# Kernel tuning notes

Measured on AMD Instinct MI355X. Metric: run time of the kernel, lower is better.

The kernel has to match this reference:

```python
import jax, jax.numpy as jnp
import numpy as np

N, E, D, ED, H, OUT = 10000, 640000, 128, 64, 8, 128  # nodes, edges, node_dim, edge_dim, heads, out_features


def _lin_init(key, out_d, in_d):
    kw, kb = jax.random.split(key)
    lim = 1.0 / np.sqrt(in_d)
    W = jax.random.uniform(kw, (out_d, in_d), jnp.float32, -lim, lim)
    b = jax.random.uniform(kb, (out_d,), jnp.float32, -lim, lim)
    return W, b


def setup_inputs() -> dict:
    key = jax.random.key(0)
    ks = jax.random.split(key, 9)
    h = jax.random.normal(ks[0], (N, D), jnp.float32)
    t_ij = jax.random.normal(ks[1], (E, ED), jnp.float32)
    edge_index = jax.random.randint(ks[2], (2, E), 0, N, dtype=jnp.int64)
    Wq, bq = _lin_init(ks[3], D, D)
    Wk, bk = _lin_init(ks[4], D, D)
    W1, b1 = _lin_init(ks[5], OUT, D)   # MLP layer 1
    W2, b2 = _lin_init(ks[6], OUT, OUT)  # MLP layer 2
    Wre, bre = _lin_init(ks[7], D, ED)
    Wc, bc = _lin_init(ks[8], OUT, OUT)  # combine_heads
    return dict(h=h, t_ij=t_ij, edge_index=edge_index, Wq=Wq, bq=bq, Wk=Wk, bk=bk,
                W1=W1, b1=b1, W2=W2, b2=b2, Wre=Wre, bre=bre, Wc=Wc, bc=bc)


def reference(h, t_ij, edge_index, Wq, bq, Wk, bk, W1, b1, W2, b2, Wre, bre, Wc, bc):
    n_j, n_i = edge_index[0], edge_index[1]
    n_nodes = h.shape[0]
    # projections on nodes, then gather per edge
    q_i = (h @ Wq.T + bq).reshape(n_nodes, H, -1)[n_i]          # [E, H, d_h]
    k_j = (h @ Wk.T + bk).reshape(n_nodes, H, -1)[n_j]          # [E, H, d_h]
    v_nodes = jax.nn.silu(h @ W1.T + b1) @ W2.T + b2            # MLP(h): [N, OUT]
    v_j = v_nodes.reshape(n_nodes, H, -1)[n_j]                  # [E, H, d_h]
    re = jax.nn.silu(t_ij @ Wre.T + bre).reshape(t_ij.shape[0], H, -1)  # [E, H, d_h]
    # per-edge attention logits fused with edge features
    a_ij = (q_i * k_j * re).sum(-1, keepdims=True)              # [E, H, 1]
    # segment softmax grouped by destination node n_i
    m = jax.ops.segment_max(a_ij, n_i, num_segments=n_nodes)
    ex = jnp.exp(a_ij - m[n_i])
    s = jax.ops.segment_sum(ex, n_i, num_segments=n_nodes)
    a_i = ex / (s[n_i] + 1e-16)
    # note: original scales AFTER softmax
    a_i = a_i * (1.0 / np.sqrt(v_j.shape[2]))
    sea_ij = (a_i * v_j).reshape(a_i.shape[0], -1)              # [E, OUT]
    sea_ij = sea_ij @ Wc.T + bc                                 # combine_heads
    return sea_ij
```

## Files before the change

kernel.cpp:

```cpp
#include <hip/hip_runtime.h>

typedef __attribute__((ext_vector_type(8))) _Float16 half8;
typedef __attribute__((ext_vector_type(4))) float floatx4;

#define NN    10000
#define EE    640000
#define DD    128
#define EDD   64
#define HH    8
#define OUTD  128

__device__ __forceinline__ float fast_rcp(float x) { return __builtin_amdgcn_rcpf(x); }

__device__ __forceinline__ half8 cvt8h(const float* __restrict__ p) {
    const floatx4 a = *(const floatx4*)(const void*)p;
    const floatx4 b = *(const floatx4*)(const void*)(p + 4);
    half8 r;
    r[0] = (_Float16)a[0]; r[1] = (_Float16)a[1];
    r[2] = (_Float16)a[2]; r[3] = (_Float16)a[3];
    r[4] = (_Float16)b[0]; r[5] = (_Float16)b[1];
    r[6] = (_Float16)b[2]; r[7] = (_Float16)b[3];
    return r;
}

__device__ __forceinline__ int idx_is64(const int* __restrict__ eidx) {
    return ((eidx[1] | eidx[3] | eidx[5] | eidx[7]) == 0) ? 1 : 0;
}

__global__ void __launch_bounds__(64) k_node(
    const float* __restrict__ h,
    const float* __restrict__ Wq, const float* __restrict__ bq,
    const float* __restrict__ Wk, const float* __restrict__ bk,
    const float* __restrict__ W1, const float* __restrict__ b1,
    const float* __restrict__ W2, const float* __restrict__ b2,
    _Float16* __restrict__ qb, _Float16* __restrict__ kb,
    _Float16* __restrict__ vb, float* __restrict__ sf)
{
    __shared__ _Float16 L[16 * 136];
    const int lane = threadIdx.x;
    const int tile = blockIdx.x;
    const int c16 = lane & 15, q4 = lane >> 4;
    const int m0 = tile * 16;

    const int tid = tile * 64 + lane;
    sf[tid] = 0.0f;
    sf[tid + 40000] = 0.0f;

    const float* hrow = h + (m0 + c16) * DD + q4 * 8;
    half8 af[4];
    af[0] = cvt8h(hrow + 0);
    af[1] = cvt8h(hrow + 32);
    af[2] = cvt8h(hrow + 64);
    af[3] = cvt8h(hrow + 96);

    for (int w = 0; w < 2; ++w) {
        const float* W  = w ? Wk : Wq;
        const float* Bv = w ? bk : bq;
        _Float16* dst   = w ? kb : qb;
        for (int nt = 0; nt < 8; ++nt) {
            const int col = nt * 16 + c16;
            const float bias = Bv[col];
            floatx4 acc = {bias, bias, bias, bias};
            const float* wr = W + col * DD + q4 * 8;
            for (int s = 0; s < 4; ++s)
                acc = __builtin_amdgcn_mfma_f32_16x16x32_f16(
                    af[s], cvt8h(wr + s * 32), acc, 0, 0, 0);
            for (int r = 0; r < 4; ++r)
                dst[(m0 + q4 * 4 + r) * DD + col] = (_Float16)acc[r];
        }
    }

    for (int nt = 0; nt < 8; ++nt) {
        const int col = nt * 16 + c16;
        const float bias = b1[col];
        floatx4 acc = {bias, bias, bias, bias};
        const float* wr = W1 + col * DD + q4 * 8;
        for (int s = 0; s < 4; ++s)
            acc = __builtin_amdgcn_mfma_f32_16x16x32_f16(
                af[s], cvt8h(wr + s * 32), acc, 0, 0, 0);
        for (int r = 0; r < 4; ++r) {
            const float x = acc[r];
            L[(q4 * 4 + r) * 136 + col] = (_Float16)(x * fast_rcp(1.0f + __expf(-x)));
        }
    }
    __syncthreads();

    half8 af2[4];
    const _Float16* l2 = L + c16 * 136 + q4 * 8;
    for (int s = 0; s < 4; ++s)
        af2[s] = *(const half8*)(const void*)(l2 + s * 32);
    for (int nt = 0; nt < 8; ++nt) {
        const int col = nt * 16 + c16;
        const float bias = b2[col];
        floatx4 acc = {bias, bias, bias, bias};
        const float* wr = W2 + col * DD + q4 * 8;
        for (int s = 0; s < 4; ++s)
            acc = __builtin_amdgcn_mfma_f32_16x16x32_f16(
                af2[s], cvt8h(wr + s * 32), acc, 0, 0, 0);
        for (int r = 0; r < 4; ++r)
            vb[(m0 + q4 * 4 + r) * DD + col] = (_Float16)acc[r];
    }
}

__global__ void __launch_bounds__(256) k_logits(
    const float* __restrict__ t, const int* __restrict__ eidx,
    const float* __restrict__ Wre, const float* __restrict__ bre,
    const _Float16* __restrict__ qb, const _Float16* __restrict__ kb,
    float* __restrict__ exf, float* __restrict__ sf)
{
    const int wave = threadIdx.x >> 6;
    const int lane = threadIdx.x & 63;
    const int c16 = lane & 15, q4 = lane >> 4;
    const int tile = blockIdx.x * 4 + wave;
    const int m0 = tile * 16;

    const int is64 = idx_is64(eidx);

    const float* trow = t + (m0 + c16) * EDD + q4 * 8;
    const half8 a0 = cvt8h(trow);
    const half8 a1 = cvt8h(trow + 32);

    int e_r[4], ni_r[4], nj_r[4];
    for (int r = 0; r < 4; ++r) {
        const int e = m0 + q4 * 4 + r;
        e_r[r] = e;
        if (is64) { nj_r[r] = eidx[2 * e];      ni_r[r] = eidx[2 * EE + 2 * e]; }
        else      { nj_r[r] = eidx[e];          ni_r[r] = eidx[EE + e]; }
    }

    for (int nt = 0; nt < 8; ++nt) {
        const int col = nt * 16 + c16;
        const float bias = bre[col];
        floatx4 acc = {bias, bias, bias, bias};
        const float* wr = Wre + col * EDD + q4 * 8;
        acc = __builtin_amdgcn_mfma_f32_16x16x32_f16(a0, cvt8h(wr), acc, 0, 0, 0);
        acc = __builtin_amdgcn_mfma_f32_16x16x32_f16(a1, cvt8h(wr + 32), acc, 0, 0, 0);

        float part[4];
        for (int r = 0; r < 4; ++r) {
            const float x = acc[r];
            const float re = x * fast_rcp(1.0f + __expf(-x));
            const float qv = (float)qb[ni_r[r] * DD + col];
            const float kv = (float)kb[nj_r[r] * DD + col];
            part[r] = re * qv * kv;
        }
        for (int m = 1; m < 16; m <<= 1) {
            part[0] += __shfl_xor(part[0], m, 64);
            part[1] += __shfl_xor(part[1], m, 64);
            part[2] += __shfl_xor(part[2], m, 64);
            part[3] += __shfl_xor(part[3], m, 64);
        }
        if (c16 < 4) {
            const int r = c16;
            const float ex = __expf(part[r]);
            exf[e_r[r] * HH + nt] = ex;
            atomicAdd(&sf[ni_r[r] * HH + nt], ex);
        }
    }
}

__global__ void __launch_bounds__(256) k_out(
    const int* __restrict__ eidx, const float* __restrict__ exf,
    const float* __restrict__ sf, const _Float16* __restrict__ vb,
    const float* __restrict__ Wc, const float* __restrict__ bc,
    float* __restrict__ outp)
{
    __shared__ float Lf[4][16 * 132];
    const int wave = threadIdx.x >> 6;
    const int lane = threadIdx.x & 63;
    const int c16 = lane & 15, q4 = lane >> 4;
    const int tile = blockIdx.x * 4 + wave;
    const int m0 = tile * 16;

    const int is64 = idx_is64(eidx);

    const int e_a = m0 + c16;
    int nj, ni;
    if (is64) { nj = eidx[2 * e_a]; ni = eidx[2 * EE + 2 * e_a]; }
    else      { nj = eidx[e_a];     ni = eidx[EE + e_a]; }

    half8 af[4];
    for (int s = 0; s < 4; ++s) {
        const int h0 = s * 2 + (q4 >> 1);
        const float exv = exf[e_a * HH + h0];
        const float sv = sf[ni * HH + h0];
        const float asc = exv * fast_rcp(sv + 1e-16f) * 0.25f;
        const half8 v8 = *(const half8*)(const void*)(vb + nj * DD + s * 32 + q4 * 8);
        half8 y;
        for (int j = 0; j < 8; ++j)
            y[j] = (_Float16)((float)v8[j] * asc);
        af[s] = y;
    }

    floatx4 acc[8];
    for (int nt = 0; nt < 8; ++nt) {
        const int col = nt * 16 + c16;
        const float bias = bc[col];
        acc[nt] = (floatx4){bias, bias, bias, bias};
        const float* wr = Wc + col * DD + q4 * 8;
        for (int s = 0; s < 4; ++s)
            acc[nt] = __builtin_amdgcn_mfma_f32_16x16x32_f16(
                af[s], cvt8h(wr + s * 32), acc[nt], 0, 0, 0);
    }

    float* Lw = Lf[wave];
    for (int nt = 0; nt < 8; ++nt)
        for (int r = 0; r < 4; ++r)
            Lw[(q4 * 4 + r) * 132 + nt * 16 + c16] = acc[nt][r];
    __syncthreads();

    float* ob = outp + (size_t)m0 * OUTD;
    for (int tt = 0; tt < 8; ++tt) {
        const int idx = tt * 64 + lane;
        const int row = idx >> 5;
        const int c4 = (idx & 31) * 4;
        const floatx4 val = *(const floatx4*)(const void*)&Lw[row * 132 + c4];
        *(floatx4*)(void*)(ob + row * OUTD + c4) = val;
    }
}

extern "C" void kernel_launch(void* const* d_in, const int* in_sizes, int n_in,
                              void* d_out, int out_size, void* d_ws, size_t ws_size,
                              hipStream_t stream) {
    (void)in_sizes; (void)n_in; (void)out_size; (void)ws_size;
    const float* h   = (const float*)d_in[0];
    const float* t   = (const float*)d_in[1];
    const int*   eidx= (const int*)d_in[2];
    const float* Wq  = (const float*)d_in[3];
    const float* bq  = (const float*)d_in[4];
    const float* Wk  = (const float*)d_in[5];
    const float* bk  = (const float*)d_in[6];
    const float* W1  = (const float*)d_in[7];
    const float* b1  = (const float*)d_in[8];
    const float* W2  = (const float*)d_in[9];
    const float* b2  = (const float*)d_in[10];
    const float* Wre = (const float*)d_in[11];
    const float* bre = (const float*)d_in[12];
    const float* Wc  = (const float*)d_in[13];
    const float* bc  = (const float*)d_in[14];
    float* out = (float*)d_out;

    char* ws = (char*)d_ws;
    _Float16* qb = (_Float16*)(ws);
    _Float16* kb = (_Float16*)(ws + 2560000);
    _Float16* vb = (_Float16*)(ws + 5120000);
    float*    exf= (float*)   (ws + 7680000);
    float*    sf = (float*)   (ws + 28160000);

    k_node<<<dim3(625), dim3(64), 0, stream>>>(h, Wq, bq, Wk, bk, W1, b1, W2, b2,
                                               qb, kb, vb, sf);
    k_logits<<<dim3(10000), dim3(256), 0, stream>>>(t, eidx, Wre, bre, qb, kb, exf, sf);
    k_out<<<dim3(10000), dim3(256), 0, stream>>>(eidx, exf, sf, vb, Wc, bc, out);
}
```

Baseline: 1.038 ms.

## Pre-convert weights to fp16, widen node kernel, prefetch q/k gathers, halve out staging

```diff
diff --git a/kernel.cpp b/kernel.cpp
--- a/kernel.cpp
+++ b/kernel.cpp
@@ -27,76 +27,94 @@
     return ((eidx[1] | eidx[3] | eidx[5] | eidx[7]) == 0) ? 1 : 0;
 }
 
-__global__ void __launch_bounds__(64) k_node(
-    const float* __restrict__ h,
-    const float* __restrict__ Wq, const float* __restrict__ bq,
-    const float* __restrict__ Wk, const float* __restrict__ bk,
-    const float* __restrict__ W1, const float* __restrict__ b1,
-    const float* __restrict__ W2, const float* __restrict__ b2,
+__global__ void __launch_bounds__(256) k_prep(
+    const float* __restrict__ Wq, const float* __restrict__ Wk,
+    const float* __restrict__ W1, const float* __restrict__ W2,
+    const float* __restrict__ Wc, const float* __restrict__ Wre,
+    _Float16* __restrict__ w16, float* __restrict__ sf)
+{
+    const int gid = blockIdx.x * 256 + threadIdx.x;
+    float v;
+    if (gid < 16384)      v = Wq[gid];
+    else if (gid < 32768) v = Wk[gid - 16384];
+    else if (gid < 49152) v = W1[gid - 32768];
+    else if (gid < 65536) v = W2[gid - 49152];
+    else if (gid < 81920) v = Wc[gid - 65536];
+    else                  v = Wre[gid - 81920];
+    w16[gid] = (_Float16)v;
+    if (gid < 80000) sf[gid] = 0.0f;
+}
+
+__global__ void __launch_bounds__(512) k_node(
+    const float* __restrict__ h, const _Float16* __restrict__ w16,
+    const float* __restrict__ bq, const float* __restrict__ bk,
+    const float* __restrict__ b1, const float* __restrict__ b2,
     _Float16* __restrict__ qb, _Float16* __restrict__ kb,
-    _Float16* __restrict__ vb, float* __restrict__ sf)
+    _Float16* __restrict__ vb)
 {
     __shared__ _Float16 L[16 * 136];
-    const int lane = threadIdx.x;
-    const int tile = blockIdx.x;
+    const int wave = threadIdx.x >> 6;
+    const int lane = threadIdx.x & 63;
     const int c16 = lane & 15, q4 = lane >> 4;
-    const int m0 = tile * 16;
-
-    const int tid = tile * 64 + lane;
-    sf[tid] = 0.0f;
-    sf[tid + 40000] = 0.0f;
+    const int m0 = blockIdx.x * 16;
+
+    const _Float16* Wq16 = w16;
+    const _Float16* Wk16 = w16 + 16384;
+    const _Float16* W116 = w16 + 32768;
+    const _Float16* W216 = w16 + 49152;
 
     const float* hrow = h + (m0 + c16) * DD + q4 * 8;
     half8 af[4];
-    af[0] = cvt8h(hrow + 0);
+    af[0] = cvt8h(hrow);
     af[1] = cvt8h(hrow + 32);
     af[2] = cvt8h(hrow + 64);
     af[3] = cvt8h(hrow + 96);
 
-    for (int w = 0; w < 2; ++w) {
-        const float* W  = w ? Wk : Wq;
-        const float* Bv = w ? bk : bq;
-        _Float16* dst   = w ? kb : qb;
-        for (int nt = 0; nt < 8; ++nt) {
-            const int col = nt * 16 + c16;
-            const float bias = Bv[col];
-            floatx4 acc = {bias, bias, bias, bias};
-            const float* wr = W + col * DD + q4 * 8;
-            for (int s = 0; s < 4; ++s)
-                acc = __builtin_amdgcn_mfma_f32_16x16x32_f16(
-                    af[s], cvt8h(wr + s * 32), acc, 0, 0, 0);
+#pragma unroll
+    for (int i = 0; i < 3; ++i) {
+        const int u = wave * 3 + i;
+        const int pass = u >> 3;
+        const int nt = u & 7;
+        const _Float16* W = (pass == 0) ? Wq16 : ((pass == 1) ? Wk16 : W116);
+        const float* B    = (pass == 0) ? bq   : ((pass == 1) ? bk   : b1);
+        const int col = nt * 16 + c16;
+        const float bias = B[col];
+        floatx4 acc = {bias, bias, bias, bias};
+        const _Float16* wr = W + col * DD + q4 * 8;
+#pragma unroll
+        for (int s = 0; s < 4; ++s)
+            acc = __builtin_amdgcn_mfma_f32_16x16x32_f16(
+                af[s], *(const half8*)(const void*)(wr + s * 32), acc, 0, 0, 0);
+        if (pass < 2) {
+            _Float16* dst = pass ? kb : qb;
+#pragma unroll
             for (int r = 0; r < 4; ++r)
                 dst[(m0 + q4 * 4 + r) * DD + col] = (_Float16)acc[r];
-        }
-    }
-
-    for (int nt = 0; nt < 8; ++nt) {
-        const int col = nt * 16 + c16;
-        const float bias = b1[col];
+        } else {
+#pragma unroll
+            for (int r = 0; r < 4; ++r) {
+                const float x = acc[r];
+                L[(q4 * 4 + r) * 136 + col] = (_Float16)(x * fast_rcp(1.0f + __expf(-x)));
+            }
+        }
+    }
+    __syncthreads();
+
+    half8 af2[4];
+    const _Float16* l2 = L + c16 * 136 + q4 * 8;
+#pragma unroll
+    for (int s = 0; s < 4; ++s)
+        af2[s] = *(const half8*)(const void*)(l2 + s * 32);
+    {
+        const int col = wave * 16 + c16;
+        const float bias = b2[col];
         floatx4 acc = {bias, bias, bias, bias};
-        const float* wr = W1 + col * DD + q4 * 8;
+        const _Float16* wr = W216 + col * DD + q4 * 8;
+#pragma unroll
         for (int s = 0; s < 4; ++s)
             acc = __builtin_amdgcn_mfma_f32_16x16x32_f16(
-                af[s], cvt8h(wr + s * 32), acc, 0, 0, 0);
-        for (int r = 0; r < 4; ++r) {
-            const float x = acc[r];
-            L[(q4 * 4 + r) * 136 + col] = (_Float16)(x * fast_rcp(1.0f + __expf(-x)));
-        }
-    }
-    __syncthreads();
-
-    half8 af2[4];
-    const _Float16* l2 = L + c16 * 136 + q4 * 8;
-    for (int s = 0; s < 4; ++s)
-        af2[s] = *(const half8*)(const void*)(l2 + s * 32);
-    for (int nt = 0; nt < 8; ++nt) {
-        const int col = nt * 16 + c16;
-        const float bias = b2[col];
-        floatx4 acc = {bias, bias, bias, bias};
-        const float* wr = W2 + col * DD + q4 * 8;
-        for (int s = 0; s < 4; ++s)
-            acc = __builtin_amdgcn_mfma_f32_16x16x32_f16(
-                af2[s], cvt8h(wr + s * 32), acc, 0, 0, 0);
+                af2[s], *(const half8*)(const void*)(wr + s * 32), acc, 0, 0, 0);
+#pragma unroll
         for (int r = 0; r < 4; ++r)
             vb[(m0 + q4 * 4 + r) * DD + col] = (_Float16)acc[r];
     }
@@ -104,7 +122,7 @@
 
 __global__ void __launch_bounds__(256) k_logits(
     const float* __restrict__ t, const int* __restrict__ eidx,
-    const float* __restrict__ Wre, const float* __restrict__ bre,
+    const _Float16* __restrict__ Wre16, const float* __restrict__ bre,
     const _Float16* __restrict__ qb, const _Float16* __restrict__ kb,
     float* __restrict__ exf, float* __restrict__ sf)
 {
@@ -120,29 +138,47 @@
     const half8 a0 = cvt8h(trow);
     const half8 a1 = cvt8h(trow + 32);
 
-    int e_r[4], ni_r[4], nj_r[4];
+    int e_r[4], ni_r[4];
+    const _Float16* qrow[4];
+    const _Float16* krow[4];
+#pragma unroll
     for (int r = 0; r < 4; ++r) {
         const int e = m0 + q4 * 4 + r;
-        e_r[r] = e;
-        if (is64) { nj_r[r] = eidx[2 * e];      ni_r[r] = eidx[2 * EE + 2 * e]; }
-        else      { nj_r[r] = eidx[e];          ni_r[r] = eidx[EE + e]; }
-    }
+        int nj, ni;
+        if (is64) { nj = eidx[2 * e];      ni = eidx[2 * EE + 2 * e]; }
+        else      { nj = eidx[e];          ni = eidx[EE + e]; }
+        e_r[r] = e; ni_r[r] = ni;
+        qrow[r] = qb + ni * DD + c16;
+        krow[r] = kb + nj * DD + c16;
+    }
+
+    _Float16 qv[4], kv[4], qn[4], kn[4];
+#pragma unroll
+    for (int r = 0; r < 4; ++r) { qv[r] = qrow[r][0]; kv[r] = krow[r][0]; }
 
     for (int nt = 0; nt < 8; ++nt) {
+        if (nt < 7) {
+#pragma unroll
+            for (int r = 0; r < 4; ++r) {
+                qn[r] = qrow[r][(nt + 1) * 16];
+                kn[r] = krow[r][(nt + 1) * 16];
+            }
+        }
         const int col = nt * 16 + c16;
         const float bias = bre[col];
         floatx4 acc = {bias, bias, bias, bias};
-        const float* wr = Wre + col * EDD + q4 * 8;
-        acc = __builtin_amdgcn_mfma_f32_16x16x32_f16(a0, cvt8h(wr), acc, 0, 0, 0);
-        acc = __builtin_amdgcn_mfma_f32_16x16x32_f16(a1, cvt8h(wr + 32), acc, 0, 0, 0);
+        const _Float16* wr = Wre16 + col * EDD + q4 * 8;
+        acc = __builtin_amdgcn_mfma_f32_16x16x32_f16(
+            a0, *(const half8*)(const void*)wr, acc, 0, 0, 0);
+        acc = __builtin_amdgcn_mfma_f32_16x16x32_f16(
+            a1, *(const half8*)(const void*)(wr + 32), acc, 0, 0, 0);
 
         float part[4];
+#pragma unroll
         for (int r = 0; r < 4; ++r) {
             const float x = acc[r];
             const float re = x * fast_rcp(1.0f + __expf(-x));
-            const float qv = (float)qb[ni_r[r] * DD + col];
-            const float kv = (float)kb[nj_r[r] * DD + col];
-            part[r] = re * qv * kv;
+            part[r] = re * (float)qv[r] * (float)kv[r];
         }
         for (int m = 1; m < 16; m <<= 1) {
             part[0] += __shfl_xor(part[0], m, 64);
@@ -156,16 +192,18 @@
             exf[e_r[r] * HH + nt] = ex;
             atomicAdd(&sf[ni_r[r] * HH + nt], ex);
         }
-    }
-}
-
-__global__ void __launch_bounds__(256) k_out(
+#pragma unroll
+        for (int r = 0; r < 4; ++r) { qv[r] = qn[r]; kv[r] = kn[r]; }
+    }
+}
+
+__global__ void __launch_bounds__(256, 8) k_out(
     const int* __restrict__ eidx, const float* __restrict__ exf,
     const float* __restrict__ sf, const _Float16* __restrict__ vb,
-    const float* __restrict__ Wc, const float* __restrict__ bc,
+    const _Float16* __restrict__ Wc16, const float* __restrict__ bc,
     float* __restrict__ outp)
 {
-    __shared__ float Lf[4][16 * 132];
+    __shared__ float Lf[4][16 * 68];
     const int wave = threadIdx.x >> 6;
     const int lane = threadIdx.x & 63;
     const int c16 = lane & 15, q4 = lane >> 4;
@@ -180,6 +218,7 @@
     else      { nj = eidx[e_a];     ni = eidx[EE + e_a]; }
 
     half8 af[4];
+#pragma unroll
     for (int s = 0; s < 4; ++s) {
         const int h0 = s * 2 + (q4 >> 1);
         const float exv = exf[e_a * HH + h0];
@@ -187,35 +226,42 @@
         const float asc = exv * fast_rcp(sv + 1e-16f) * 0.25f;
         const half8 v8 = *(const half8*)(const void*)(vb + nj * DD + s * 32 + q4 * 8);
         half8 y;
+#pragma unroll
         for (int j = 0; j < 8; ++j)
             y[j] = (_Float16)((float)v8[j] * asc);
         af[s] = y;
     }
 
     floatx4 acc[8];
+#pragma unroll
     for (int nt = 0; nt < 8; ++nt) {
         const int col = nt * 16 + c16;
         const float bias = bc[col];
         acc[nt] = (floatx4){bias, bias, bias, bias};
-        const float* wr = Wc + col * DD + q4 * 8;
+        const _Float16* wr = Wc16 + col * DD + q4 * 8;
+#pragma unroll
         for (int s = 0; s < 4; ++s)
             acc[nt] = __builtin_amdgcn_mfma_f32_16x16x32_f16(
-                af[s], cvt8h(wr + s * 32), acc[nt], 0, 0, 0);
+                af[s], *(const half8*)(const void*)(wr + s * 32), acc[nt], 0, 0, 0);
     }
 
     float* Lw = Lf[wave];
-    for (int nt = 0; nt < 8; ++nt)
-        for (int r = 0; r < 4; ++r)
-            Lw[(q4 * 4 + r) * 132 + nt * 16 + c16] = acc[nt][r];
-    __syncthreads();
-
     float* ob = outp + (size_t)m0 * OUTD;
-    for (int tt = 0; tt < 8; ++tt) {
-        const int idx = tt * 64 + lane;
-        const int row = idx >> 5;
-        const int c4 = (idx & 31) * 4;
-        const floatx4 val = *(const floatx4*)(const void*)&Lw[row * 132 + c4];
-        *(floatx4*)(void*)(ob + row * OUTD + c4) = val;
+#pragma unroll
+    for (int p = 0; p < 2; ++p) {
+#pragma unroll
+        for (int j = 0; j < 4; ++j)
+#pragma unroll
+            for (int r = 0; r < 4; ++r)
+                Lw[(q4 * 4 + r) * 68 + j * 16 + c16] = acc[p * 4 + j][r];
+#pragma unroll
+        for (int tt = 0; tt < 4; ++tt) {
+            const int idx = tt * 64 + lane;
+            const int row = idx >> 4;
+            const int c4 = (idx & 15) * 4;
+            const floatx4 val = *(const floatx4*)(const void*)&Lw[row * 68 + c4];
+            *(floatx4*)(void*)(ob + row * OUTD + p * 64 + c4) = val;
+        }
     }
 }
 
@@ -246,9 +292,10 @@
     _Float16* vb = (_Float16*)(ws + 5120000);
     float*    exf= (float*)   (ws + 7680000);
     float*    sf = (float*)   (ws + 28160000);
-
-    k_node<<<dim3(625), dim3(64), 0, stream>>>(h, Wq, bq, Wk, bk, W1, b1, W2, b2,
-                                               qb, kb, vb, sf);
-    k_logits<<<dim3(10000), dim3(256), 0, stream>>>(t, eidx, Wre, bre, qb, kb, exf, sf);
-    k_out<<<dim3(10000), dim3(256), 0, stream>>>(eidx, exf, sf, vb, Wc, bc, out);
-}
+    _Float16* w16= (_Float16*)(ws + 28480000);
+
+    k_prep<<<dim3(352), dim3(256), 0, stream>>>(Wq, Wk, W1, W2, Wc, Wre, w16, sf);
+    k_node<<<dim3(625), dim3(512), 0, stream>>>(h, w16, bq, bk, b1, b2, qb, kb, vb);
+    k_logits<<<dim3(10000), dim3(256), 0, stream>>>(t, eidx, w16 + 81920, bre, qb, kb, exf, sf);
+    k_out<<<dim3(10000), dim3(256), 0, stream>>>(eidx, exf, sf, vb, w16 + 65536, bc, out);
+}
```

Result: faster. 886.0 us (-14.6%).
